# Performance work log

Hardware: AMD Instinct MI355X
Metric: run time of the kernel (lower is better)

The kernel has to match this reference:

```python
import math
import jax, jax.numpy as jnp
import numpy as np

NUM_BITS = 8
NUM_CHUNKS = 16
EPS = 1e-5


def quantize_ste(x, mn, mx, num_bits=NUM_BITS):
    """Uniform affine quantize with straight-through estimator (repo's UniformQuantize,
    enforce_true_zero=False). mn/mx are treated as constants (repo casts to float())."""
    mn = jax.lax.stop_gradient(mn)
    mx = jax.lax.stop_gradient(mx)
    qmax = 2.0 ** num_bits - 1.0
    scale = jnp.maximum((mx - mn) / qmax, 1e-8)
    q = jnp.round(jnp.clip((x - mn) / scale, 0.0, qmax)) * scale + mn
    return x + jax.lax.stop_gradient(q - x)


def quant_measure(x):
    """QuantMeasure in training mode: min/max = mean over batch of per-sample min/max."""
    xf = jax.lax.stop_gradient(x.reshape(x.shape[0], -1))
    mn = xf.min(axis=-1).mean()
    mx = xf.max(axis=-1).mean()
    return quantize_ste(x, mn, mx, NUM_BITS)


def qconv2d(x, w, b, stride, padding, groups):
    """QConv2d forward: quantize input (QuantMeasure), weight and bias (per-tensor min/max),
    then standard conv. Grad quantization / biprecision only affects backward numerics."""
    qx = quant_measure(x)
    qw = quantize_ste(w, w.min(), w.max(), NUM_BITS)
    out = jax.lax.conv_general_dilated(
        qx, qw, window_strides=(stride, stride),
        padding=[(padding, padding), (padding, padding)],
        feature_group_count=groups,
        dimension_numbers=('NCHW', 'OIHW', 'NCHW'))
    if b is not None:
        qb = quantize_ste(b, b.min(), b.max(), NUM_BITS)
        out = out + qb[None, :, None, None]
    return out


def range_bn(x, weight, bias):
    """RangeBN (training mode): range-based scale estimate over NUM_CHUNKS chunks."""
    x = quant_measure(x)
    B, C, H, W = x.shape
    y = jnp.transpose(x, (1, 0, 2, 3)).reshape(C, NUM_CHUNKS, -1)  # [C, chunks, BHW/chunks]
    mean_max = y.max(axis=-1).mean(axis=-1)   # [C]
    mean_min = y.min(axis=-1).mean(axis=-1)   # [C]
    mean = y.reshape(C, -1).mean(axis=-1)     # [C]
    n = y.shape[-1]
    scale_fix = (0.5 * 0.35) * (1 + (math.pi * math.log(4)) ** 0.5) / ((2 * math.log(n)) ** 0.5)
    scale = 1.0 / ((mean_max - mean_min) * scale_fix + EPS)
    scale = quantize_ste(scale, scale.min(), scale.max(), NUM_BITS)
    out = (x - mean[None, :, None, None]) * scale[None, :, None, None]
    qw = quantize_ste(weight, weight.min(), weight.max(), NUM_BITS)
    out = out * qw[None, :, None, None]
    out = out + bias[None, :, None, None]
    return out


def setup_inputs() -> dict:
    key = jax.random.key(0)
    ks = jax.random.split(key, 8)
    B, Cin, Cout, H, W, K = 32, 256, 256, 56, 56, 3
    x = jax.random.normal(ks[0], (B, Cin, H, W), dtype=jnp.float32)
    # depthwise conv: groups=Cin -> weight [Cin, 1, K, K], kaiming-ish scale
    dw_w = jax.random.normal(ks[1], (Cin, 1, K, K), dtype=jnp.float32) * (1.0 / K)
    dw_b = jax.random.normal(ks[2], (Cin,), dtype=jnp.float32) * 0.1
    bn1_w = jax.random.uniform(ks[3], (Cin,), dtype=jnp.float32)
    bn1_b = jnp.zeros((Cin,), dtype=jnp.float32)
    # pointwise conv: [Cout, Cin, 1, 1], bias=False
    pw_w = jax.random.normal(ks[4], (Cout, Cin, 1, 1), dtype=jnp.float32) * (1.0 / math.sqrt(Cin))
    bn2_w = jax.random.uniform(ks[5], (Cout,), dtype=jnp.float32)
    bn2_b = jnp.zeros((Cout,), dtype=jnp.float32)
    return {"x": x, "dw_w": dw_w, "dw_b": dw_b, "bn1_w": bn1_w, "bn1_b": bn1_b,
            "pw_w": pw_w, "bn2_w": bn2_w, "bn2_b": bn2_b}


def reference(x, dw_w, dw_b, bn1_w, bn1_b, pw_w, bn2_w, bn2_b):
    Cin = x.shape[1]
    h = qconv2d(x, dw_w, dw_b, stride=1, padding=1, groups=Cin)  # depthwise QConv2d
    h = jax.nn.relu(range_bn(h, bn1_w, bn1_b))
    h = qconv2d(h, pw_w, None, stride=1, padding=0, groups=1)    # pointwise QConv2d (no bias)
    h = jax.nn.relu(range_bn(h, bn2_w, bn2_b))
    return h
```

## Files before the change

### kernel.cpp

```cpp
#include <hip/hip_runtime.h>
#include <math.h>

#define IMG 56
#define HW 3136
#define NCH 256
#define NB 32
#define SAMPLE (NCH*HW)
#define TOT (NB*SAMPLE)
#define ASTR 68

typedef int i32x4 __attribute__((ext_vector_type(4)));


__device__ __forceinline__ float qz(float x, float mn, float scale) {
    float t = (x - mn) / scale;
    t = fminf(fmaxf(t, 0.f), 255.f);
    return rintf(t) * scale + mn;
}

__device__ __forceinline__ float codef(float x, float mn, float scale) {
    return rintf(fminf(fmaxf((x - mn) / scale, 0.f), 255.f));
}

__device__ __forceinline__ unsigned enc(float f) {
    unsigned u = __float_as_uint(f);
    return (u & 0x80000000u) ? ~u : (u ^ 0x80000000u);
}
__device__ __forceinline__ float dec(unsigned u) {
    unsigned v = (u & 0x80000000u) ? (u ^ 0x80000000u) : ~u;
    return __uint_as_float(v);
}

__device__ __forceinline__ void blk_red_minmax(float& mn, float& mx) {
    __shared__ float smn[4], smx[4];
    __syncthreads();
    #pragma unroll
    for (int o = 32; o > 0; o >>= 1) {
        mn = fminf(mn, __shfl_down(mn, o));
        mx = fmaxf(mx, __shfl_down(mx, o));
    }
    int lane = threadIdx.x & 63, w = threadIdx.x >> 6;
    if (lane == 0) { smn[w] = mn; smx[w] = mx; }
    __syncthreads();
    if (threadIdx.x == 0) {
        int nw = (int)blockDim.x >> 6;
        for (int i = 1; i < nw; i++) { mn = fminf(mn, smn[i]); mx = fmaxf(mx, smx[i]); }
    }
}

__device__ __forceinline__ void blk_red_minmax_bcast(float& mn, float& mx) {
    __shared__ float bb[2];
    blk_red_minmax(mn, mx);
    if (threadIdx.x == 0) { bb[0] = mn; bb[1] = mx; }
    __syncthreads();
    mn = bb[0]; mx = bb[1];
}

__device__ __forceinline__ float blk_red_sum(float v) {
    __shared__ float ss[4];
    __syncthreads();
    #pragma unroll
    for (int o = 32; o > 0; o >>= 1) v += __shfl_down(v, o);
    int lane = threadIdx.x & 63, w = threadIdx.x >> 6;
    if (lane == 0) ss[w] = v;
    __syncthreads();
    if (threadIdx.x == 0) {
        int nw = (int)blockDim.x >> 6;
        for (int i = 1; i < nw; i++) v += ss[i];
    }
    return v;
}


__global__ void k_init(unsigned* xsl, unsigned* pwsl, unsigned* o2mn, unsigned* o2mx, float* o2sum) {
    int i = blockIdx.x * 256 + threadIdx.x;
    o2mn[i] = 0xFFFFFFFFu; o2mx[i] = 0u; o2sum[i] = 0.f;
    if (blockIdx.x == 0) {
        if (threadIdx.x < 64) xsl[threadIdx.x] = (threadIdx.x < 32) ? 0xFFFFFFFFu : 0u;
        if (threadIdx.x == 64) { pwsl[0] = 0xFFFFFFFFu; pwsl[1] = 0u; }
    }
}

__global__ __launch_bounds__(256) void k_front(const float4* __restrict__ x4, const float4* __restrict__ pw4,
                                               unsigned* xsl, unsigned* pwsl) {
    int id = blockIdx.x;
    if (id < 512) {
        int b = id >> 4, blk = id & 15;
        const float4* p = x4 + (size_t)b * 200704 + (size_t)blk * 12544;
        float mn = INFINITY, mx = -INFINITY;
        for (int k = threadIdx.x; k < 12544; k += 256) {
            float4 v = p[k];
            mn = fminf(mn, fminf(fminf(v.x, v.y), fminf(v.z, v.w)));
            mx = fmaxf(mx, fmaxf(fmaxf(v.x, v.y), fmaxf(v.z, v.w)));
        }
        blk_red_minmax(mn, mx);
        if (threadIdx.x == 0) {
            atomicMin(&xsl[b], enc(mn));
            atomicMax(&xsl[32 + b], enc(mx));
        }
    } else {
        int i = (id - 512) * 256 + threadIdx.x;
        float4 v = pw4[i];
        float mn = fminf(fminf(v.x, v.y), fminf(v.z, v.w));
        float mx = fmaxf(fmaxf(v.x, v.y), fmaxf(v.z, v.w));
        blk_red_minmax(mn, mx);
        if (threadIdx.x == 0) { atomicMin(&pwsl[0], enc(mn)); atomicMax(&pwsl[1], enc(mx)); }
    }
}

__global__ void k_fin1(const float* __restrict__ dww, const float* __restrict__ dwb,
                       const unsigned* __restrict__ xsl, const unsigned* __restrict__ pwsl, float* sc) {
    int tid = threadIdx.x;
    float mn = INFINITY, mx = -INFINITY;
    #pragma unroll
    for (int i = 0; i < 9; i++) {
        int idx = i * 256 + tid;
        if (idx < 2304) { float v = dww[idx]; mn = fminf(mn, v); mx = fmaxf(mx, v); }
    }
    blk_red_minmax(mn, mx);
    float w1min = mn, w1max = mx;
    float v = dwb[tid]; mn = v; mx = v;
    blk_red_minmax(mn, mx);
    if (tid == 0) {
        float sm = 0.f, sx = 0.f;
        for (int i = 0; i < 32; i++) { sm += dec(xsl[i]); sx += dec(xsl[32 + i]); }
        float m = sm / 32.f, X = sx / 32.f;
        sc[0] = m;      sc[1] = fmaxf((X - m) / 255.f, 1e-8f);
        sc[2] = w1min;  sc[3] = fmaxf((w1max - w1min) / 255.f, 1e-8f);
        sc[4] = mn;     sc[5] = fmaxf((mx - mn) / 255.f, 1e-8f);
        float pmn = dec(pwsl[0]), pmx = dec(pwsl[1]);
        sc[10] = pmn; sc[11] = fmaxf((pmx - pmn) / 255.f, 1e-8f);
    }
}

__global__ __launch_bounds__(256) void k_qw(const float* __restrict__ pw, const float* __restrict__ sc,
                                            char* __restrict__ wcodes, float* __restrict__ Wsum) {
    int co = blockIdx.x, ci = threadIdx.x;
    float kw = codef(pw[co * 256 + ci], sc[10], sc[11]);
    wcodes[co * 256 + ci] = (char)((int)kw - 128);
    float s = blk_red_sum(kw);
    if (ci == 0) Wsum[co] = s;
}

__global__ __launch_bounds__(256) void k_dwconv(const float4* __restrict__ x4, const float* __restrict__ w,
                                                const float* __restrict__ bias, float* __restrict__ h1,
                                                const float* __restrict__ sc,
                                                float* __restrict__ h1mn, float* __restrict__ h1mx,
                                                float* __restrict__ h1sm) {
    int bc = blockIdx.x, c = bc & 255;
    __shared__ float tile[58 * 68];
    int tid = threadIdx.x;
    if (tid < 228) {
        int row, col2;
        if (tid < 58)       { row = 0;              col2 = 3 + tid; }
        else if (tid < 116) { row = 57;             col2 = 3 + tid - 58; }
        else if (tid < 172) { row = 1 + tid - 116;  col2 = 3; }
        else                { row = 1 + tid - 172;  col2 = 60; }
        tile[row * 68 + col2] = 0.f;
    }
    float mnx = sc[0], scx = sc[1];
    const float4* px = x4 + (size_t)bc * 784;
    #pragma unroll
    for (int it = 0; it < 4; it++) {
        int idx = it * 256 + tid;
        if (idx < 784) {
            int i = idx / 14, j = (idx - i * 14) * 4;
            float4 v = px[idx];
            v.x = qz(v.x, mnx, scx); v.y = qz(v.y, mnx, scx);
            v.z = qz(v.z, mnx, scx); v.w = qz(v.w, mnx, scx);
            *(float4*)&tile[(i + 1) * 68 + j + 4] = v;
        }
    }
    __syncthreads();
    float qw[9];
    #pragma unroll
    for (int k = 0; k < 9; k++) qw[k] = qz(w[c * 9 + k], sc[2], sc[3]);
    float qb = qz(bias[c], sc[4], sc[5]);
    float4* po = (float4*)(h1 + (size_t)bc * HW);
    float lmn = INFINITY, lmx = -INFINITY, lsum = 0.f;
    #pragma unroll
    for (int it = 0; it < 4; it++) {
        int idx = it * 256 + tid;
        if (idx < 784) {
            int i = idx / 14, j = (idx - i * 14) * 4;
            float o0 = qb, o1 = qb, o2v = qb, o3 = qb;
            #pragma unroll
            for (int r = 0; r < 3; r++) {
                const float* row = &tile[(i + r) * 68 + j + 3];
                float a0 = row[0];
                float4 mid = *(const float4*)&row[1];
                float a5 = row[5];
                float w0 = qw[3 * r], w1 = qw[3 * r + 1], w2 = qw[3 * r + 2];
                o0  += a0    * w0 + mid.x * w1 + mid.y * w2;
                o1  += mid.x * w0 + mid.y * w1 + mid.z * w2;
                o2v += mid.y * w0 + mid.z * w1 + mid.w * w2;
                o3  += mid.z * w0 + mid.w * w1 + a5    * w2;
            }
            po[idx] = make_float4(o0, o1, o2v, o3);
            lmn = fminf(lmn, fminf(fminf(o0, o1), fminf(o2v, o3)));
            lmx = fmaxf(lmx, fmaxf(fmaxf(o0, o1), fmaxf(o2v, o3)));
            lsum += (o0 + o1) + (o2v + o3);
        }
    }
    blk_red_minmax(lmn, lmx);
    float ls = blk_red_sum(lsum);
    if (tid == 0) { h1mn[bc] = lmn; h1mx[bc] = lmx; h1sm[bc] = ls; }
}

__global__ __launch_bounds__(256) void k_stats1(const float* __restrict__ h1mn, const float* __restrict__ h1mx,
                                                const float* __restrict__ h1sm,
                                                const float* __restrict__ bn1w, const float* __restrict__ bn1b,
                                                float* sc,
                                                float* __restrict__ A2v, float* __restrict__ B2v) {
    int tid = threadIdx.x, lane = tid & 63, w = tid >> 6;
    __shared__ float bmn[32], bmx[32], sp[4], lP[256], lQ[256];
    #pragma unroll
    for (int i = 0; i < 8; i++) {
        int b = w * 8 + i;
        float4 m4 = *(const float4*)&h1mn[b * 256 + lane * 4];
        float4 x4 = *(const float4*)&h1mx[b * 256 + lane * 4];
        float mn = fminf(fminf(m4.x, m4.y), fminf(m4.z, m4.w));
        float mx = fmaxf(fmaxf(x4.x, x4.y), fmaxf(x4.z, x4.w));
        #pragma unroll
        for (int o = 32; o > 0; o >>= 1) { mn = fminf(mn, __shfl_down(mn, o)); mx = fmaxf(mx, __shfl_down(mx, o)); }
        if (lane == 0) { bmn[b] = mn; bmx[b] = mx; }
    }
    __syncthreads();
    if (tid == 0) {
        float sm = 0.f, sx = 0.f;
        for (int i = 0; i < 32; i++) { sm += bmn[i]; sx += bmx[i]; }
        float m = sm / 32.f, X = sx / 32.f;
        sp[0] = m; sp[1] = fmaxf((X - m) / 255.f, 1e-8f);
        sc[6] = sp[0]; sc[7] = sp[1];
        sc[14] = 1.f / sp[1];
        sc[15] = -sp[0] / sp[1];
    }
    __syncthreads();
    float mn1 = sp[0], s1 = sp[1];
    int c = tid;
    float mmax = 0.f, mmin = 0.f, sum = 0.f;
    #pragma unroll
    for (int ck = 0; ck < 16; ck++) {
        float c0n = h1mn[(2 * ck) * 256 + c], c1n = h1mn[(2 * ck + 1) * 256 + c];
        float c0x = h1mx[(2 * ck) * 256 + c], c1x = h1mx[(2 * ck + 1) * 256 + c];
        mmin += qz(fminf(c0n, c1n), mn1, s1);
        mmax += qz(fmaxf(c0x, c1x), mn1, s1);
        sum  += h1sm[(2 * ck) * 256 + c] + h1sm[(2 * ck + 1) * 256 + c];
    }
    mmin *= 0.0625f; mmax *= 0.0625f;
    float mean = sum / 100352.f;
    const float scale_fix = (float)(0.175 * (1.0 + sqrt(3.14159265358979323846 * log(4.0))) / sqrt(2.0 * log(6272.0)));
    float scale = 1.f / ((mmax - mmin) * scale_fix + 1e-5f);
    float ssn = scale, ssx = scale;
    blk_red_minmax_bcast(ssn, ssx);
    float wv = bn1w[c];
    float wmn = wv, wmx = wv;
    blk_red_minmax_bcast(wmn, wmx);
    float qs = qz(scale, ssn, fmaxf((ssx - ssn) / 255.f, 1e-8f));
    float qw = qz(wv, wmn, fmaxf((wmx - wmn) / 255.f, 1e-8f));
    float a1 = qs * qw;
    float be = bn1b[c] - mean * a1;
    float p1v = s1 * a1, q1v = mn1 * a1 + be;
    lP[c] = p1v; lQ[c] = q1v;
    __syncthreads();
    #pragma unroll
    for (int i = 0; i < 8; i++) {
        int b = w * 8 + i;
        float4 m4 = *(const float4*)&h1mn[b * 256 + lane * 4];
        float4 x4 = *(const float4*)&h1mx[b * 256 + lane * 4];
        float mn = INFINITY, mx = -INFINITY;
        #pragma unroll
        for (int j = 0; j < 4; j++) {
            int cc = lane * 4 + j;
            float kn = rintf(fminf(fmaxf(((&m4.x)[j] - mn1) / s1, 0.f), 255.f));
            float kx = rintf(fminf(fmaxf(((&x4.x)[j] - mn1) / s1, 0.f), 255.f));
            float hn = fmaxf(kn * lP[cc] + lQ[cc], 0.f);
            float hx = fmaxf(kx * lP[cc] + lQ[cc], 0.f);
            mn = fminf(mn, hn); mx = fmaxf(mx, hx);
        }
        #pragma unroll
        for (int o = 32; o > 0; o >>= 1) { mn = fminf(mn, __shfl_down(mn, o)); mx = fmaxf(mx, __shfl_down(mx, o)); }
        if (lane == 0) { bmn[b] = mn; bmx[b] = mx; }
    }
    __syncthreads();
    if (tid == 0) {
        float sm = 0.f, sx = 0.f;
        for (int i = 0; i < 32; i++) { sm += bmn[i]; sx += bmx[i]; }
        float m = sm / 32.f, X = sx / 32.f;
        sp[2] = m; sp[3] = fmaxf((X - m) / 255.f, 1e-8f);
        sc[8] = sp[2]; sc[9] = sp[3];
    }
    __syncthreads();
    A2v[c] = lP[c] / sp[3];
    B2v[c] = (lQ[c] - sp[2]) / sp[3];
}

__global__ __launch_bounds__(256) void k_gemm(const float* __restrict__ h1, const char* __restrict__ wcodes,
                                              const float* __restrict__ Wsum, const float* __restrict__ sc,
                                              const float* __restrict__ A2v, const float* __restrict__ B2v,
                                              float* __restrict__ o2,
                                              unsigned* o2mn, unsigned* o2mx, float* o2sum) {
    int b = blockIdx.y, p0 = blockIdx.x * 64;
    __shared__ unsigned AsU[64 * ASTR];
    __shared__ float BpW[4][64];
    __shared__ float BpT[64];
    int tid = threadIdx.x, lane = tid & 63, w = tid >> 6;
    int col = lane & 15, quad = lane >> 4;
    float A1 = sc[14], B1 = sc[15];
    const float* colp = h1 + (size_t)b * SAMPLE + p0 + lane;
    unsigned base = lane * ASTR + 16 * w;
    float bp = 0.f;
    #pragma unroll 4
    for (int t2 = 0; t2 < 16; t2++) {
        int ci = 64 * w + 4 * t2;
        float v0 = colp[(size_t)ci * HW];
        float v1 = colp[(size_t)(ci + 1) * HW];
        float v2 = colp[(size_t)(ci + 2) * HW];
        float v3 = colp[(size_t)(ci + 3) * HW];
        float k0f = rintf(fminf(fmaxf(fmaf(v0, A1, B1), 0.f), 255.f));
        float k1f = rintf(fminf(fmaxf(fmaf(v1, A1, B1), 0.f), 255.f));
        float k2f = rintf(fminf(fmaxf(fmaf(v2, A1, B1), 0.f), 255.f));
        float k3f = rintf(fminf(fmaxf(fmaf(v3, A1, B1), 0.f), 255.f));
        float c0 = rintf(fminf(fmaxf(fmaf(k0f, A2v[ci],     B2v[ci]),     0.f), 255.f));
        float c1 = rintf(fminf(fmaxf(fmaf(k1f, A2v[ci + 1], B2v[ci + 1]), 0.f), 255.f));
        float c2 = rintf(fminf(fmaxf(fmaf(k2f, A2v[ci + 2], B2v[ci + 2]), 0.f), 255.f));
        float c3 = rintf(fminf(fmaxf(fmaf(k3f, A2v[ci + 3], B2v[ci + 3]), 0.f), 255.f));
        bp += (c0 + c1) + (c2 + c3);
        unsigned b0 = (unsigned)(((int)c0 - 128) & 0xFF);
        unsigned b1 = (unsigned)(((int)c1 - 128) & 0xFF);
        unsigned b2 = (unsigned)(((int)c2 - 128) & 0xFF);
        unsigned b3 = (unsigned)(((int)c3 - 128) & 0xFF);
        AsU[base + t2] = b0 | (b1 << 8) | (b2 << 16) | (b3 << 24);
    }
    BpW[w][lane] = bp;
    __syncthreads();
    const char* wb = wcodes + (size_t)(w * 64 + col) * 256 + quad * 16;
    i32x4 acc[4][4];
    #pragma unroll
    for (int i = 0; i < 4; i++)
        #pragma unroll
        for (int j = 0; j < 4; j++) acc[i][j] = (i32x4){0, 0, 0, 0};
    i32x4 bcur[4];
    #pragma unroll
    for (int nt = 0; nt < 4; nt++) bcur[nt] = *(const i32x4*)(wb + (size_t)nt * 4096);
    for (int step = 0; step < 4; step++) {
        i32x4 af[4];
        #pragma unroll
        for (int mt = 0; mt < 4; mt++)
            af[mt] = *(const i32x4*)&AsU[(size_t)(mt * 16 + col) * ASTR + step * 16 + quad * 4];
        i32x4 bnx[4];
        if (step < 3) {
            #pragma unroll
            for (int nt = 0; nt < 4; nt++) bnx[nt] = *(const i32x4*)(wb + (size_t)nt * 4096 + (step + 1) * 64);
        }
        #pragma unroll
        for (int mt = 0; mt < 4; mt++)
            #pragma unroll
            for (int nt = 0; nt < 4; nt++)
                acc[mt][nt] = __builtin_amdgcn_mfma_i32_16x16x64_i8(af[mt], bcur[nt], acc[mt][nt], 0, 0, 0);
        if (step < 3) {
            #pragma unroll
            for (int nt = 0; nt < 4; nt++) bcur[nt] = bnx[nt];
        }
    }
    if (tid < 64) BpT[tid] = BpW[0][tid] + BpW[1][tid] + BpW[2][tid] + BpW[3][tid];
    __syncthreads();
    float alpha = sc[11] * sc[9];
    float beta  = sc[11] * sc[8] + 128.f * alpha;
    float gamma = sc[10] * sc[9] + 128.f * alpha;
    float delta = 256.f * sc[10] * sc[8] - 4194304.f * alpha;
    float Wv[4];
    #pragma unroll
    for (int nt = 0; nt < 4; nt++) Wv[nt] = Wsum[w * 64 + nt * 16 + col];
    float snn[4], sxx[4], ssm[4];
    #pragma unroll
    for (int nt = 0; nt < 4; nt++) { snn[nt] = INFINITY; sxx[nt] = -INFINITY; ssm[nt] = 0.f; }
    float* obase = o2 + ((size_t)b * HW + p0) * 256 + w * 64 + col;
    #pragma unroll
    for (int mt = 0; mt < 4; mt++) {
        float bp4[4];
        #pragma unroll
        for (int r = 0; r < 4; r++) bp4[r] = BpT[mt * 16 + quad * 4 + r];
        #pragma unroll
        for (int nt = 0; nt < 4; nt++) {
            float wterm = beta * Wv[nt] + delta;
            #pragma unroll
            for (int r = 0; r < 4; r++) {
                float val = alpha * (float)acc[mt][nt][r] + gamma * bp4[r] + wterm;
                obase[(size_t)(mt * 16 + quad * 4 + r) * 256 + nt * 16] = val;
                snn[nt] = fminf(snn[nt], val);
                sxx[nt] = fmaxf(sxx[nt], val);
                ssm[nt] += val;
            }
        }
    }
    #pragma unroll
    for (int nt = 0; nt < 4; nt++) {
        snn[nt] = fminf(snn[nt], __shfl_xor(snn[nt], 16));
        sxx[nt] = fmaxf(sxx[nt], __shfl_xor(sxx[nt], 16));
        ssm[nt] += __shfl_xor(ssm[nt], 16);
        snn[nt] = fminf(snn[nt], __shfl_xor(snn[nt], 32));
        sxx[nt] = fmaxf(sxx[nt], __shfl_xor(sxx[nt], 32));
        ssm[nt] += __shfl_xor(ssm[nt], 32);
    }
    if (lane < 16) {
        #pragma unroll
        for (int nt = 0; nt < 4; nt++) {
            int idx = b * 256 + w * 64 + nt * 16 + lane;
            atomicMin(&o2mn[idx], enc(snn[nt]));
            atomicMax(&o2mx[idx], enc(sxx[nt]));
            atomicAdd(&o2sum[idx], ssm[nt]);
        }
    }
}

__global__ __launch_bounds__(256) void k_stats2(const unsigned* __restrict__ o2mnU, const unsigned* __restrict__ o2mxU,
                                                const float* __restrict__ o2sm,
                                                const float* __restrict__ bn2w, const float* __restrict__ bn2b,
                                                float* sc, float* __restrict__ P2, float* __restrict__ Q2) {
    int tid = threadIdx.x, lane = tid & 63, w = tid >> 6;
    __shared__ float bmn[32], bmx[32], sp[2];
    #pragma unroll
    for (int i = 0; i < 8; i++) {
        int b = w * 8 + i;
        uint4 um = *(const uint4*)&o2mnU[b * 256 + lane * 4];
        uint4 ux = *(const uint4*)&o2mxU[b * 256 + lane * 4];
        float mn = fminf(fminf(dec(um.x), dec(um.y)), fminf(dec(um.z), dec(um.w)));
        float mx = fmaxf(fmaxf(dec(ux.x), dec(ux.y)), fmaxf(dec(ux.z), dec(ux.w)));
        #pragma unroll
        for (int o = 32; o > 0; o >>= 1) { mn = fminf(mn, __shfl_down(mn, o)); mx = fmaxf(mx, __shfl_down(mx, o)); }
        if (lane == 0) { bmn[b] = mn; bmx[b] = mx; }
    }
    __syncthreads();
    if (tid == 0) {
        float sm = 0.f, sx = 0.f;
        for (int i = 0; i < 32; i++) { sm += bmn[i]; sx += bmx[i]; }
        float m = sm / 32.f, X = sx / 32.f;
        sp[0] = m; sp[1] = fmaxf((X - m) / 255.f, 1e-8f);
        sc[12] = sp[0]; sc[13] = sp[1];
    }
    __syncthreads();
    float mno = sp[0], so = sp[1];
    int c = tid;
    float mmax = 0.f, mmin = 0.f, sum = 0.f;
    #pragma unroll
    for (int ck = 0; ck < 16; ck++) {
        float c0n = dec(o2mnU[(2 * ck) * 256 + c]), c1n = dec(o2mnU[(2 * ck + 1) * 256 + c]);
        float c0x = dec(o2mxU[(2 * ck) * 256 + c]), c1x = dec(o2mxU[(2 * ck + 1) * 256 + c]);
        mmin += qz(fminf(c0n, c1n), mno, so);
        mmax += qz(fmaxf(c0x, c1x), mno, so);
        sum  += o2sm[(2 * ck) * 256 + c] + o2sm[(2 * ck + 1) * 256 + c];
    }
    mmin *= 0.0625f; mmax *= 0.0625f;
    float mean = sum / 100352.f;
    const float scale_fix = (float)(0.175 * (1.0 + sqrt(3.14159265358979323846 * log(4.0))) / sqrt(2.0 * log(6272.0)));
    float scale = 1.f / ((mmax - mmin) * scale_fix + 1e-5f);
    float ssn = scale, ssx = scale;
    blk_red_minmax_bcast(ssn, ssx);
    float wv = bn2w[c];
    float wmn = wv, wmx = wv;
    blk_red_minmax_bcast(wmn, wmx);
    float qs = qz(scale, ssn, fmaxf((ssx - ssn) / 255.f, 1e-8f));
    float qw = qz(wv, wmn, fmaxf((wmx - wmn) / 255.f, 1e-8f));
    float a2 = qs * qw;
    float be = bn2b[c] - mean * a2;
    P2[c] = so * a2; Q2[c] = mno * a2 + be;
}

__global__ __launch_bounds__(256) void k_apply(const float* __restrict__ o2, const float* __restrict__ sc,
                                               const float* __restrict__ P2, const float* __restrict__ Q2,
                                               float* __restrict__ out) {
    __shared__ float tile[64][65];
    int b = blockIdx.z, p0 = blockIdx.x * 64, co0 = blockIdx.y * 64;
    int t = threadIdx.x, rr = t >> 4, cq = t & 15;
    float mno = sc[12], so = sc[13];
    #pragma unroll
    for (int it = 0; it < 4; it++) {
        int p = rr + 16 * it;
        float4 v = *(const float4*)&o2[((size_t)b * HW + p0 + p) * 256 + co0 + cq * 4];
        *(float4*)&tile[p][cq * 4] = v;
    }
    __syncthreads();
    #pragma unroll
    for (int it = 0; it < 4; it++) {
        int col = rr + 16 * it;
        int c = co0 + col;
        float pv = P2[c], qv = Q2[c];
        float4 r;
        #pragma unroll
        for (int j = 0; j < 4; j++) {
            float val = tile[cq * 4 + j][col];
            (&r.x)[j] = fmaxf(rintf(fminf(fmaxf((val - mno) / so, 0.f), 255.f)) * pv + qv, 0.f);
        }
        *(float4*)&out[((size_t)b * 256 + c) * HW + p0 + cq * 4] = r;
    }
}


extern "C" void kernel_launch(void* const* d_in, const int* in_sizes, int n_in,
                              void* d_out, int out_size, void* d_ws, size_t ws_size,
                              hipStream_t stream) {
    (void)in_sizes; (void)n_in; (void)out_size; (void)ws_size;
    const float* x    = (const float*)d_in[0];
    const float* dww  = (const float*)d_in[1];
    const float* dwb  = (const float*)d_in[2];
    const float* bn1w = (const float*)d_in[3];
    const float* bn1b = (const float*)d_in[4];
    const float* pww  = (const float*)d_in[5];
    const float* bn2w = (const float*)d_in[6];
    const float* bn2b = (const float*)d_in[7];

    float* h1   = (float*)d_ws;
    float* o2   = h1 + TOT;
    float* after = o2 + TOT;
    char* wcodes = (char*)after;
    float* Wsum  = after + 16384;
    float* sc    = Wsum + 256;
    unsigned* xsl   = (unsigned*)(sc + 32);
    unsigned* pwsl  = xsl + 64;
    unsigned* o2mnU = pwsl + 64;
    unsigned* o2mxU = o2mnU + 8192;
    float* o2sm = (float*)(o2mxU + 8192);
    float* h1mn = o2sm + 8192;
    float* h1mx = h1mn + 8192;
    float* h1sm = h1mx + 8192;
    float* P2 = h1sm + 8192; float* Q2 = P2 + 256;
    float* A2v = Q2 + 256;   float* B2v = A2v + 256;

    k_init<<<32, 256, 0, stream>>>(xsl, pwsl, o2mnU, o2mxU, o2sm);
    k_front<<<576, 256, 0, stream>>>((const float4*)x, (const float4*)pww, xsl, pwsl);
    k_fin1<<<1, 256, 0, stream>>>(dww, dwb, xsl, pwsl, sc);
    k_qw<<<256, 256, 0, stream>>>(pww, sc, wcodes, Wsum);
    k_dwconv<<<NB * NCH, 256, 0, stream>>>((const float4*)x, dww, dwb, h1, sc, h1mn, h1mx, h1sm);
    k_stats1<<<1, 256, 0, stream>>>(h1mn, h1mx, h1sm, bn1w, bn1b, sc, A2v, B2v);
    k_gemm<<<dim3(49, 32), 256, 0, stream>>>(h1, wcodes, Wsum, sc, A2v, B2v, o2, o2mnU, o2mxU, o2sm);
    k_stats2<<<1, 256, 0, stream>>>(o2mnU, o2mxU, o2sm, bn2w, bn2b, sc, P2, Q2);
    k_apply<<<dim3(49, 4, 32), 256, 0, stream>>>(o2, sc, P2, Q2, (float*)d_out);
}
```

Baseline: 358.7 us.

## Recompute pointwise GEMM in apply pass instead of storing fp32 intermediate

The fp32 GEMM output no longer goes to global memory. The first GEMM pass stores the packed int8 activation codes and per-pixel code sums, and only accumulates statistics. A second kernel reloads the codes, reruns the int8 MFMA GEMM, and applies the second RangeBN quantization and ReLU directly. This cuts large fp32 write and read traffic at the cost of doing the GEMM twice, and the output stores are only 64-byte contiguous segments.

```diff
diff --git a/kernel.cpp b/kernel.cpp
--- a/kernel.cpp
+++ b/kernel.cpp
@@ -295,12 +295,12 @@
     B2v[c] = (lQ[c] - sp[2]) / sp[3];
 }
 
-__global__ __launch_bounds__(256) void k_gemm(const float* __restrict__ h1, const char* __restrict__ wcodes,
-                                              const float* __restrict__ Wsum, const float* __restrict__ sc,
-                                              const float* __restrict__ A2v, const float* __restrict__ B2v,
-                                              float* __restrict__ o2,
-                                              unsigned* o2mn, unsigned* o2mx, float* o2sum) {
-    int b = blockIdx.y, p0 = blockIdx.x * 64;
+__global__ __launch_bounds__(256) void k_gemm1(const float* __restrict__ h1, const char* __restrict__ wcodes,
+                                               const float* __restrict__ Wsum, const float* __restrict__ sc,
+                                               const float* __restrict__ A2v, const float* __restrict__ B2v,
+                                               unsigned* __restrict__ blob, float* __restrict__ BpG,
+                                               unsigned* o2mn, unsigned* o2mx, float* o2sum) {
+    int b = blockIdx.y, pt = blockIdx.x, p0 = pt * 64;
     __shared__ unsigned AsU[64 * ASTR];
     __shared__ float BpW[4][64];
     __shared__ float BpT[64];
@@ -334,6 +334,18 @@
     }
     BpW[w][lane] = bp;
     __syncthreads();
+    unsigned bbase = (unsigned)(b * 49 + pt) * 4096;
+    #pragma unroll
+    for (int i = 0; i < 16; i++) {
+        int idx = i * 256 + tid;
+        blob[bbase + idx] = AsU[(idx >> 6) * ASTR + (idx & 63)];
+    }
+    if (tid < 64) {
+        float s = BpW[0][tid] + BpW[1][tid] + BpW[2][tid] + BpW[3][tid];
+        BpT[tid] = s;
+        BpG[(size_t)b * HW + p0 + tid] = s;
+    }
+    __syncthreads();
     const char* wb = wcodes + (size_t)(w * 64 + col) * 256 + quad * 16;
     i32x4 acc[4][4];
     #pragma unroll
@@ -363,8 +375,6 @@
             for (int nt = 0; nt < 4; nt++) bcur[nt] = bnx[nt];
         }
     }
-    if (tid < 64) BpT[tid] = BpW[0][tid] + BpW[1][tid] + BpW[2][tid] + BpW[3][tid];
-    __syncthreads();
     float alpha = sc[11] * sc[9];
     float beta  = sc[11] * sc[8] + 128.f * alpha;
     float gamma = sc[10] * sc[9] + 128.f * alpha;
@@ -375,7 +385,6 @@
     float snn[4], sxx[4], ssm[4];
     #pragma unroll
     for (int nt = 0; nt < 4; nt++) { snn[nt] = INFINITY; sxx[nt] = -INFINITY; ssm[nt] = 0.f; }
-    float* obase = o2 + ((size_t)b * HW + p0) * 256 + w * 64 + col;
     #pragma unroll
     for (int mt = 0; mt < 4; mt++) {
         float bp4[4];
@@ -387,7 +396,6 @@
             #pragma unroll
             for (int r = 0; r < 4; r++) {
                 float val = alpha * (float)acc[mt][nt][r] + gamma * bp4[r] + wterm;
-                obase[(size_t)(mt * 16 + quad * 4 + r) * 256 + nt * 16] = val;
                 snn[nt] = fminf(snn[nt], val);
                 sxx[nt] = fmaxf(sxx[nt], val);
                 ssm[nt] += val;
@@ -467,32 +475,87 @@
     P2[c] = so * a2; Q2[c] = mno * a2 + be;
 }
 
-__global__ __launch_bounds__(256) void k_apply(const float* __restrict__ o2, const float* __restrict__ sc,
+__global__ __launch_bounds__(256) void k_gemm2(const unsigned* __restrict__ blob, const char* __restrict__ wcodes,
+                                               const float* __restrict__ Wsum, const float* __restrict__ BpG,
+                                               const float* __restrict__ sc,
                                                const float* __restrict__ P2, const float* __restrict__ Q2,
                                                float* __restrict__ out) {
-    __shared__ float tile[64][65];
-    int b = blockIdx.z, p0 = blockIdx.x * 64, co0 = blockIdx.y * 64;
-    int t = threadIdx.x, rr = t >> 4, cq = t & 15;
+    int b = blockIdx.y, pt = blockIdx.x, p0 = pt * 64;
+    __shared__ unsigned smem[64 * ASTR];
+    float* sT = (float*)smem;
+    int tid = threadIdx.x, lane = tid & 63, w = tid >> 6;
+    int col = lane & 15, quad = lane >> 4;
+    const unsigned* ab = blob + (size_t)((unsigned)(b * 49 + pt)) * 4096;
+    #pragma unroll
+    for (int i = 0; i < 16; i++) {
+        int idx = i * 256 + tid;
+        smem[(idx >> 6) * ASTR + (idx & 63)] = ab[idx];
+    }
+    __syncthreads();
+    const char* wb = wcodes + (size_t)(w * 64 + col) * 256 + quad * 16;
+    i32x4 acc[4][4];
+    #pragma unroll
+    for (int i = 0; i < 4; i++)
+        #pragma unroll
+        for (int j = 0; j < 4; j++) acc[i][j] = (i32x4){0, 0, 0, 0};
+    i32x4 bcur[4];
+    #pragma unroll
+    for (int nt = 0; nt < 4; nt++) bcur[nt] = *(const i32x4*)(wb + (size_t)nt * 4096);
+    for (int step = 0; step < 4; step++) {
+        i32x4 af[4];
+        #pragma unroll
+        for (int mt = 0; mt < 4; mt++)
+            af[mt] = *(const i32x4*)&smem[(size_t)(mt * 16 + col) * ASTR + step * 16 + quad * 4];
+        i32x4 bnx[4];
+        if (step < 3) {
+            #pragma unroll
+            for (int nt = 0; nt < 4; nt++) bnx[nt] = *(const i32x4*)(wb + (size_t)nt * 4096 + (step + 1) * 64);
+        }
+        #pragma unroll
+        for (int mt = 0; mt < 4; mt++)
+            #pragma unroll
+            for (int nt = 0; nt < 4; nt++)
+                acc[mt][nt] = __builtin_amdgcn_mfma_i32_16x16x64_i8(af[mt], bcur[nt], acc[mt][nt], 0, 0, 0);
+        if (step < 3) {
+            #pragma unroll
+            for (int nt = 0; nt < 4; nt++) bcur[nt] = bnx[nt];
+        }
+    }
+    float alpha = sc[11] * sc[9];
+    float beta  = sc[11] * sc[8] + 128.f * alpha;
+    float gamma = sc[10] * sc[9] + 128.f * alpha;
+    float delta = 256.f * sc[10] * sc[8] - 4194304.f * alpha;
     float mno = sc[12], so = sc[13];
-    #pragma unroll
-    for (int it = 0; it < 4; it++) {
-        int p = rr + 16 * it;
-        float4 v = *(const float4*)&o2[((size_t)b * HW + p0 + p) * 256 + co0 + cq * 4];
-        *(float4*)&tile[p][cq * 4] = v;
-    }
-    __syncthreads();
-    #pragma unroll
-    for (int it = 0; it < 4; it++) {
-        int col = rr + 16 * it;
-        int c = co0 + col;
-        float pv = P2[c], qv = Q2[c];
-        float4 r;
-        #pragma unroll
-        for (int j = 0; j < 4; j++) {
-            float val = tile[cq * 4 + j][col];
-            (&r.x)[j] = fmaxf(rintf(fminf(fmaxf((val - mno) / so, 0.f), 255.f)) * pv + qv, 0.f);
-        }
-        *(float4*)&out[((size_t)b * 256 + c) * HW + p0 + cq * 4] = r;
+    float Wv[4], bpv[4][4];
+    #pragma unroll
+    for (int nt = 0; nt < 4; nt++) Wv[nt] = Wsum[w * 64 + nt * 16 + col];
+    #pragma unroll
+    for (int mt = 0; mt < 4; mt++)
+        #pragma unroll
+        for (int r = 0; r < 4; r++) bpv[mt][r] = BpG[(size_t)b * HW + p0 + mt * 16 + quad * 4 + r];
+    int co_g = tid >> 4, pl = tid & 15;
+    #pragma unroll
+    for (int mt = 0; mt < 4; mt++) {
+        __syncthreads();
+        #pragma unroll
+        for (int nt = 0; nt < 4; nt++) {
+            float wterm = beta * Wv[nt] + delta;
+            #pragma unroll
+            for (int r = 0; r < 4; r++) {
+                float val = alpha * (float)acc[mt][nt][r] + gamma * bpv[mt][r] + wterm;
+                sT[(quad * 4 + r) * 260 + w * 64 + nt * 16 + col] = val;
+            }
+        }
+        __syncthreads();
+        float* orow = out + (size_t)b * SAMPLE + (size_t)0 * HW + p0 + mt * 16 + pl;
+        #pragma unroll
+        for (int ii = 0; ii < 16; ii++) {
+            int co = ii * 16 + co_g;
+            float val = sT[pl * 260 + co];
+            float k2 = rintf(fminf(fmaxf((val - mno) / so, 0.f), 255.f));
+            float ov = fmaxf(k2 * P2[co] + Q2[co], 0.f);
+            orow[(size_t)co * HW] = ov;
+        }
     }
 }
 
@@ -511,11 +574,12 @@
     const float* bn2b = (const float*)d_in[7];
 
     float* h1   = (float*)d_ws;
-    float* o2   = h1 + TOT;
-    float* after = o2 + TOT;
+    unsigned* blob = (unsigned*)(h1 + TOT);
+    float* after = (float*)(blob + TOT / 4);
     char* wcodes = (char*)after;
     float* Wsum  = after + 16384;
-    float* sc    = Wsum + 256;
+    float* BpG   = Wsum + 256;
+    float* sc    = BpG + 100352;
     unsigned* xsl   = (unsigned*)(sc + 32);
     unsigned* pwsl  = xsl + 64;
     unsigned* o2mnU = pwsl + 64;
@@ -533,7 +597,7 @@
     k_qw<<<256, 256, 0, stream>>>(pww, sc, wcodes, Wsum);
     k_dwconv<<<NB * NCH, 256, 0, stream>>>((const float4*)x, dww, dwb, h1, sc, h1mn, h1mx, h1sm);
     k_stats1<<<1, 256, 0, stream>>>(h1mn, h1mx, h1sm, bn1w, bn1b, sc, A2v, B2v);
-    k_gemm<<<dim3(49, 32), 256, 0, stream>>>(h1, wcodes, Wsum, sc, A2v, B2v, o2, o2mnU, o2mxU, o2sm);
+    k_gemm1<<<dim3(49, 32), 256, 0, stream>>>(h1, wcodes, Wsum, sc, A2v, B2v, blob, BpG, o2mnU, o2mxU, o2sm);
     k_stats2<<<1, 256, 0, stream>>>(o2mnU, o2mxU, o2sm, bn2w, bn2b, sc, P2, Q2);
-    k_apply<<<dim3(49, 4, 32), 256, 0, stream>>>(o2, sc, P2, Q2, (float*)d_out);
-}
+    k_gemm2<<<dim3(49, 32), 256, 0, stream>>>(blob, wcodes, Wsum, BpG, sc, P2, Q2, (float*)d_out);
+}
```

Result: slower. 380.2 us (+6.0%).
